# Kernel tuning notes

Hardware: AMD Instinct MI355X
Metric: run time of the kernel (lower is better)

The kernel has to match this reference:

```python
import jax, jax.numpy as jnp
import numpy as np

HIDDEN = 4096
NUM_HEADS = 32
NUM_KV_HEADS = 8
HEAD_DIM = 128
EPS = 1e-6
ROPE_THETA = 1000000.0
B, S = 4, 1024


def setup_inputs() -> dict:
    key = jax.random.key(0)
    ks = jax.random.split(key, 8)
    sd = 1.0 / np.sqrt(HIDDEN)
    return {
        "hidden_states": jax.random.normal(ks[0], (B, S, HIDDEN), jnp.float32),
        "positions": jnp.broadcast_to(jnp.arange(S, dtype=jnp.int32), (B, S)),
        "wq": jax.random.normal(ks[1], (HIDDEN, NUM_HEADS * HEAD_DIM), jnp.float32) * sd,
        "wk": jax.random.normal(ks[2], (HIDDEN, NUM_KV_HEADS * HEAD_DIM), jnp.float32) * sd,
        "wv": jax.random.normal(ks[3], (HIDDEN, NUM_KV_HEADS * HEAD_DIM), jnp.float32) * sd,
        "wo": jax.random.normal(ks[4], (NUM_HEADS * HEAD_DIM, HIDDEN), jnp.float32) * sd,
        "q_norm_scale": jnp.ones((HEAD_DIM,), jnp.float32),
        "k_norm_scale": jnp.ones((HEAD_DIM,), jnp.float32),
    }


def _rms_norm(x, scale):
    # per-head RMSNorm over last dim (head_dim)
    var = jnp.mean(jnp.square(x), axis=-1, keepdims=True)
    return x * jax.lax.rsqrt(var + EPS) * scale


def _rope_non_neox(x, positions):
    # x: [B, S, H, D]; non-neox (interleaved) RoPE over full head_dim
    inv_freq = 1.0 / (ROPE_THETA ** (jnp.arange(0, HEAD_DIM, 2, dtype=jnp.float32) / HEAD_DIM))
    freqs = positions.astype(jnp.float32)[..., None] * inv_freq  # [B, S, D/2]
    cos = jnp.cos(freqs)[:, :, None, :]  # [B, S, 1, D/2]
    sin = jnp.sin(freqs)[:, :, None, :]
    x1 = x[..., 0::2]
    x2 = x[..., 1::2]
    o1 = x1 * cos - x2 * sin
    o2 = x2 * cos + x1 * sin
    return jnp.stack([o1, o2], axis=-1).reshape(x.shape)


def reference(hidden_states, positions, wq, wk, wv, wo, q_norm_scale, k_norm_scale):
    b, s, _ = hidden_states.shape
    q = (hidden_states @ wq).reshape(b, s, NUM_HEADS, HEAD_DIM)
    k = (hidden_states @ wk).reshape(b, s, NUM_KV_HEADS, HEAD_DIM)
    v = (hidden_states @ wv).reshape(b, s, NUM_KV_HEADS, HEAD_DIM)

    q = _rms_norm(q, q_norm_scale)
    k = _rms_norm(k, k_norm_scale)

    q = _rope_non_neox(q, positions)
    k = _rope_non_neox(k, positions)

    # GQA: expand kv heads to match q heads
    group = NUM_HEADS // NUM_KV_HEADS
    k = jnp.repeat(k, group, axis=2)  # [B, S, NH, D]
    v = jnp.repeat(v, group, axis=2)

    scale = HEAD_DIM ** -0.5
    scores = jnp.einsum("bqhd,bkhd->bhqk", q, k) * scale  # [B, NH, S, S]
    causal = jnp.tril(jnp.ones((s, s), dtype=bool))
    scores = jnp.where(causal, scores, jnp.finfo(scores.dtype).min)
    probs = jax.nn.softmax(scores, axis=-1)
    attn = jnp.einsum("bhqk,bkhd->bqhd", probs, v).reshape(b, s, NUM_HEADS * HEAD_DIM)
    return attn @ wo
```

## Files before the change

### kernel.cpp

```cpp
#include <hip/hip_runtime.h>
#include <hip/hip_bf16.h>
#include <cstdint>

#define HIDDEN 4096
#define NQ 32
#define NKV 8
#define HD 128
#define BB 4
#define SS 1024
#define NTOK (BB*SS)
#define NQKV 6144

typedef __bf16 bf16x8 __attribute__((ext_vector_type(8)));
typedef float f32x4 __attribute__((ext_vector_type(4)));
typedef unsigned short u16;
typedef unsigned int u32;

__device__ __forceinline__ void gload_lds16(const void* g, void* l) {
  __builtin_amdgcn_global_load_lds((const __attribute__((address_space(1))) u32*)g,
                                   (__attribute__((address_space(3))) u32*)l, 16, 0, 0);
}

__device__ __forceinline__ u16 f2bf(float f) {
  u32 x = __float_as_uint(f);
  u32 r = x + 0x7fffu + ((x >> 16) & 1u);
  return (u16)(r >> 16);
}
__device__ __forceinline__ float bf2f(u16 x) {
  u32 v = ((u32)x) << 16;
  return __uint_as_float(v);
}

__global__ void cast_f32_bf16_k(const float4* __restrict__ in, ushort4* __restrict__ out, int n4)
{
  for (int i = blockIdx.x*blockDim.x + threadIdx.x; i < n4; i += gridDim.x*blockDim.x) {
    float4 v = in[i];
    ushort4 o;
    o.x = f2bf(v.x); o.y = f2bf(v.y); o.z = f2bf(v.z); o.w = f2bf(v.w);
    out[i] = o;
  }
}

__global__ __launch_bounds__(256) void transpose_cast(const float* __restrict__ in,
                                                      u16* __restrict__ out, int K, int N)
{
  __shared__ float tile[32][33];
  int n0 = blockIdx.x*32, k0 = blockIdx.y*32;
  int tx = threadIdx.x & 31, ty = threadIdx.x >> 5;
  #pragma unroll
  for (int i=0;i<4;i++) {
    int k = ty + i*8;
    tile[k][tx] = in[(size_t)(k0+k)*N + n0 + tx];
  }
  __syncthreads();
  #pragma unroll
  for (int i=0;i<4;i++) {
    int n = ty + i*8;
    out[(size_t)(n0+n)*K + k0 + tx] = f2bf(tile[tx][n]);
  }
}

__global__ void rope_tab_k(const int* __restrict__ pos, float2* __restrict__ tab)
{
  int i = blockIdx.x*256 + threadIdx.x;
  if (i >= NTOK*64) return;
  int t = i >> 6, j = i & 63;
  float p = (float)pos[t];
  const float l2t = 19.931568569324174f;
  float inv = exp2f(-(float)j * (l2t/64.0f));
  float f = p * inv;
  tab[i] = make_float2(cosf(f), sinf(f));
}

template<int BF16_OUT>
__global__ __launch_bounds__(512, 2) void gemm8p(const u16* __restrict__ A,
                                                 const u16* __restrict__ Bt,
                                                 void* __restrict__ Cv,
                                                 int M, int N, int K)
{
  __shared__ u16 lA[2][2][128*64];
  __shared__ u16 lB[2][2][128*64];
  const int m0 = blockIdx.y*256, n0 = blockIdx.x*256;
  const int tid = threadIdx.x;
  const int w = tid >> 6, l = tid & 63;
  const int wm = w >> 2, wn = w & 3;
  const int cl = l & 15, g4 = l >> 4;
  const int sr = l >> 3;
  const int sg = (l & 7) ^ sr;
  const u16* Ab = A  + (size_t)m0*K;
  const u16* Bb = Bt + (size_t)n0*K;

  f32x4 acc[8][4] = {};
  const int nt = K >> 6;

#define STG_A(buf, half, kt) do { \
    gload_lds16(Ab + (size_t)((half)*128 +      w*8 + sr)*K + (kt)*64 + sg*8, &lA[buf][half][(     w*8)*64]); \
    gload_lds16(Ab + (size_t)((half)*128 + 64 + w*8 + sr)*K + (kt)*64 + sg*8, &lA[buf][half][(64 + w*8)*64]); \
  } while(0)
#define STG_B(buf, half, kt) do { \
    gload_lds16(Bb + (size_t)((half)*128 +      w*8 + sr)*K + (kt)*64 + sg*8, &lB[buf][half][(     w*8)*64]); \
    gload_lds16(Bb + (size_t)((half)*128 + 64 + w*8 + sr)*K + (kt)*64 + sg*8, &lB[buf][half][(64 + w*8)*64]); \
  } while(0)

#define RD_A(dst, buf, half) \
    _Pragma("unroll") for (int fi=0;fi<4;fi++) { \
      const int ra = (wm*64 + fi*16 + cl)*64; \
      _Pragma("unroll") for (int kk=0;kk<2;kk++) \
        dst[fi][kk] = *(const bf16x8*)&lA[buf][half][ra + (((kk*4+g4) ^ (cl&7)))*8]; \
    }
#define RD_B(dst, buf, half) \
    _Pragma("unroll") for (int fj=0;fj<2;fj++) { \
      const int rb = (wn*32 + fj*16 + cl)*64; \
      _Pragma("unroll") for (int kk=0;kk<2;kk++) \
        dst[fj][kk] = *(const bf16x8*)&lB[buf][half][rb + (((kk*4+g4) ^ (cl&7)))*8]; \
    }
#define MFMA_Q(ai, aj, afrag, bfrag) \
    __builtin_amdgcn_s_setprio(1); \
    _Pragma("unroll") for (int fi=0;fi<4;fi++) \
      _Pragma("unroll") for (int fj=0;fj<2;fj++) \
        _Pragma("unroll") for (int kk=0;kk<2;kk++) \
          acc[(ai)+fi][(aj)+fj] = __builtin_amdgcn_mfma_f32_16x16x32_bf16(afrag[fi][kk], bfrag[fj][kk], acc[(ai)+fi][(aj)+fj], 0,0,0); \
    __builtin_amdgcn_s_setprio(0);
#define BAR() { __builtin_amdgcn_s_barrier(); __builtin_amdgcn_sched_barrier(0); }

  STG_A(0,0,0); STG_B(0,0,0); STG_A(0,1,0); STG_B(0,1,0);
  asm volatile("s_waitcnt vmcnt(4)" ::: "memory");
  BAR();

  for (int t = 0; t < nt; ++t) {
    const int cur = t & 1, nxt = cur ^ 1;
    const int kn = t + 1;
    const bool pf = (kn < nt);
    bf16x8 aF[4][2], bL[2][2], bH[2][2];

    RD_A(aF, cur, 0);
    RD_B(bL, cur, 0);
    if (pf) STG_A(nxt, 0, kn);
    BAR();
    MFMA_Q(0, 0, aF, bL);
    if (pf) { asm volatile("s_waitcnt vmcnt(2)" ::: "memory"); }
    else    { asm volatile("s_waitcnt vmcnt(0)" ::: "memory"); }
    BAR();

    RD_B(bH, cur, 1);
    if (pf) STG_B(nxt, 0, kn);
    BAR();
    MFMA_Q(0, 2, aF, bH);
    BAR();

    RD_A(aF, cur, 1);
    if (pf) STG_A(nxt, 1, kn);
    BAR();
    MFMA_Q(4, 2, aF, bH);
    BAR();

    if (pf) STG_B(nxt, 1, kn);
    BAR();
    MFMA_Q(4, 0, aF, bL);
    if (pf) { asm volatile("s_waitcnt vmcnt(4)" ::: "memory"); }
    BAR();
  }
#undef STG_A
#undef STG_B
#undef RD_A
#undef RD_B
#undef MFMA_Q
#undef BAR

  #pragma unroll
  for (int am=0;am<8;am++)
    #pragma unroll
    for (int rg=0;rg<4;rg++) {
      const size_t row = m0 + (am>>2)*128 + wm*64 + (am&3)*16 + g4*4 + rg;
      #pragma unroll
      for (int an=0;an<4;an++) {
        const size_t col = n0 + (an>>1)*128 + wn*32 + (an&1)*16 + cl;
        if (BF16_OUT) ((u16*)Cv)[row*N + col] = f2bf(acc[am][an][rg]);
        else          ((float*)Cv)[row*N + col] = acc[am][an][rg];
      }
    }
}

__global__ __launch_bounds__(256) void norm_rope(u16* __restrict__ qkv,
                                                 const float* __restrict__ qsc,
                                                 const float* __restrict__ ksc,
                                                 const float2* __restrict__ tab)
{
  const int t = blockIdx.x;
  const int w = threadIdx.x >> 6, l = threadIdx.x & 63;
  const float2 cs = tab[t*64 + l];
  for (int slot = w; slot < 40; slot += 4) {
    const float* sc = (slot < 32) ? qsc : ksc;
    int col = (slot < 32) ? slot*HD : 4096 + (slot-32)*HD;
    u32* p = (u32*)(qkv + (size_t)t*NQKV + col) + l;
    u32 v = *p;
    float x0 = bf2f((u16)(v & 0xffff)), x1 = bf2f((u16)(v >> 16));
    float ss = x0*x0 + x1*x1;
    ss += __shfl_xor(ss, 1);  ss += __shfl_xor(ss, 2);  ss += __shfl_xor(ss, 4);
    ss += __shfl_xor(ss, 8);  ss += __shfl_xor(ss, 16); ss += __shfl_xor(ss, 32);
    float r = rsqrtf(ss * (1.0f/128.0f) + 1e-6f);
    float y0 = x0 * r * sc[2*l], y1 = x1 * r * sc[2*l+1];
    float o0 = y0*cs.x - y1*cs.y;
    float o1 = y1*cs.x + y0*cs.y;
    *p = (u32)f2bf(o0) | ((u32)f2bf(o1) << 16);
  }
}

__global__ __launch_bounds__(256) void v_transpose(const u16* __restrict__ qkv,
                                                   u16* __restrict__ vt)
{
  __shared__ u16 tile[32][136];
  const int s0 = blockIdx.x*32;
  const int z  = blockIdx.y;
  const int b = z >> 3, kvh = z & 7;
  const int tid = threadIdx.x;
  const int tr = tid >> 4, ln = tid & 15;
  const size_t base = ((size_t)b*SS)*NQKV + 5120 + (size_t)kvh*HD;
  #pragma unroll
  for (int i=0;i<2;i++) {
    int srow = tr + i*16;
    *(bf16x8*)&tile[srow][ln*8] =
        *(const bf16x8*)&qkv[base + (size_t)(s0+srow)*NQKV + ln*8];
  }
  __syncthreads();
  const int dr = tid >> 1, sh = (tid & 1)*16;
  u16 tmp[16];
  #pragma unroll
  for (int j=0;j<16;j++) tmp[j] = tile[sh+j][dr];
  u16* o = vt + ((size_t)z*HD + dr)*SS + s0 + sh;
  *(bf16x8*)o       = *(const bf16x8*)&tmp[0];
  *(bf16x8*)(o + 8) = *(const bf16x8*)&tmp[8];
}

__global__ __launch_bounds__(256, 2) void attn_fwd(const u16* __restrict__ qkv,
                                                   const u16* __restrict__ vt,
                                                   u16* __restrict__ out)
{
  __shared__ u16 Kb[2][64*128];
  __shared__ u16 Vb[2][128*64];
  __shared__ u16 Pl[4][16*64];
  const int qp = blockIdx.x, h = blockIdx.y, b = blockIdx.z;
  const int kvh = h >> 2;
  const int tid = threadIdx.x, w = tid >> 6, l = tid & 63;
  const int cl = l & 15, g4 = l >> 4;
  const float csc = 1.4426950408889634f * 0.08838834764831845f;
  const size_t kbase = ((size_t)b*SS)*NQKV + 4096 + (size_t)kvh*HD;
  const size_t vbase = ((size_t)b*8 + (size_t)kvh)*HD*SS;
  u16* Pw = &Pl[w][0];

  const int kr_l = l >> 4, kg_l = l & 15;
  const int vr_l = l >> 3, vg_l = l & 7;

  #pragma unroll
  for (int t = 0; t < 2; ++t) {
    const int qt = t ? (15 - qp) : qp;
    const int q0 = qt*64;

    bf16x8 qf[4];
    const size_t qrow = ((size_t)b*SS + q0 + w*16 + cl)*NQKV + h*HD;
    #pragma unroll
    for (int kk=0;kk<4;kk++) qf[kk] = *(const bf16x8*)&qkv[qrow + kk*32 + g4*8];

    f32x4 O[8] = {};
    float mrow[4] = {-INFINITY,-INFINITY,-INFINITY,-INFINITY};
    float srow[4] = {0.f,0.f,0.f,0.f};

    const int nch = qt + 1;

    #pragma unroll
    for (int i=0;i<4;i++) {
      int inst = w*4 + i;
      int r = inst*4 + kr_l;
      int g = kg_l ^ (r & 15);
      gload_lds16(qkv + kbase + (size_t)r*NQKV + g*8, &Kb[0][inst*512]);
      int d = inst*8 + vr_l;
      int gv = vg_l ^ (d & 7);
      gload_lds16(vt + vbase + (size_t)d*SS + gv*8, &Vb[0][inst*512]);
    }
    __syncthreads();
    int cur = 0;

    for (int ch = 0; ch < nch; ++ch) {
      const int kv0 = ch*64;
      if (ch + 1 < nch) {
        const size_t knext = kbase + (size_t)(kv0+64)*NQKV;
        const size_t vnext = vbase + (size_t)(kv0+64);
        u16* Kn = &Kb[cur^1][0];
        u16* Vn = &Vb[cur^1][0];
        #pragma unroll
        for (int i=0;i<4;i++) {
          int inst = w*4 + i;
          int r = inst*4 + kr_l;
          int g = kg_l ^ (r & 15);
          gload_lds16(qkv + knext + (size_t)r*NQKV + g*8, Kn + inst*512);
          int d = inst*8 + vr_l;
          int gv = vg_l ^ (d & 7);
          gload_lds16(vt + vnext + (size_t)d*SS + gv*8, Vn + inst*512);
        }
      }
      const u16* Kt  = &Kb[cur][0];
      const u16* Vtl = &Vb[cur][0];
      f32x4 s[4] = {};
      #pragma unroll
      for (int cc=0;cc<4;cc++) {
        const int kro = (cc*16+cl)*128;
        #pragma unroll
        for (int kk=0;kk<4;kk++) {
          bf16x8 kf = *(const bf16x8*)&Kt[kro + (((kk*4+g4) ^ cl))*8];
          s[cc] = __builtin_amdgcn_mfma_f32_16x16x32_bf16(qf[kk], kf, s[cc], 0,0,0);
        }
      }
      float alpha[4];
      #pragma unroll
      for (int rg=0; rg<4; ++rg) {
        const int qr = q0 + w*16 + g4*4 + rg;
        float sv[4];
        #pragma unroll
        for (int cc=0;cc<4;cc++) {
          sv[cc] = s[cc][rg]*csc;
          if (kv0 + cc*16 + cl > qr) sv[cc] = -INFINITY;
        }
        float mx = fmaxf(fmaxf(sv[0],sv[1]), fmaxf(sv[2],sv[3]));
        mx = fmaxf(mx, __shfl_xor(mx,1));
        mx = fmaxf(mx, __shfl_xor(mx,2));
        mx = fmaxf(mx, __shfl_xor(mx,4));
        mx = fmaxf(mx, __shfl_xor(mx,8));
        float mn = fmaxf(mrow[rg], mx);
        float al = exp2f(mrow[rg] - mn);
        mrow[rg] = mn;
        float p0 = exp2f(sv[0]-mn), p1 = exp2f(sv[1]-mn);
        float p2 = exp2f(sv[2]-mn), p3 = exp2f(sv[3]-mn);
        float ps = (p0+p1)+(p2+p3);
        ps += __shfl_xor(ps,1); ps += __shfl_xor(ps,2);
        ps += __shfl_xor(ps,4); ps += __shfl_xor(ps,8);
        srow[rg] = srow[rg]*al + ps;
        alpha[rg] = al;
        const int r = g4*4+rg;
        const int rs = r*64, rx = r&7;
        float pv[4] = {p0,p1,p2,p3};
        #pragma unroll
        for (int cc=0;cc<4;cc++) {
          int c = cc*16+cl;
          Pw[rs + (((c>>3) ^ rx))*8 + (c&7)] = f2bf(pv[cc]);
        }
      }
      #pragma unroll
      for (int dc=0;dc<8;dc++)
        #pragma unroll
        for (int rg=0;rg<4;rg++) O[dc][rg] *= alpha[rg];
      #pragma unroll
      for (int cc2=0;cc2<2;cc2++) {
        bf16x8 pf = *(const bf16x8*)&Pw[cl*64 + (((cc2*4+g4) ^ (cl&7)))*8];
        #pragma unroll
        for (int dc=0;dc<8;dc++) {
          bf16x8 vf = *(const bf16x8*)&Vtl[(dc*16+cl)*64 + (((cc2*4+g4) ^ (cl&7)))*8];
          O[dc] = __builtin_amdgcn_mfma_f32_16x16x32_bf16(pf, vf, O[dc], 0,0,0);
        }
      }
      __syncthreads();
      cur ^= 1;
    }
    #pragma unroll
    for (int rg=0;rg<4;rg++) {
      float inv = 1.0f / srow[rg];
      size_t ob = ((size_t)b*SS + q0 + w*16 + g4*4 + rg)*4096 + (size_t)h*HD;
      #pragma unroll
      for (int dc=0;dc<8;dc++)
        out[ob + dc*16 + cl] = f2bf(O[dc][rg]*inv);
    }
  }
}

extern "C" void kernel_launch(void* const* d_in, const int* in_sizes, int n_in,
                              void* d_out, int out_size, void* d_ws, size_t ws_size,
                              hipStream_t stream)
{
  const float* hid = (const float*)d_in[0];
  const int*   pos = (const int*)d_in[1];
  const float* wq  = (const float*)d_in[2];
  const float* wk  = (const float*)d_in[3];
  const float* wv  = (const float*)d_in[4];
  const float* wo  = (const float*)d_in[5];
  const float* qsc = (const float*)d_in[6];
  const float* ksc = (const float*)d_in[7];

  char* ws = (char*)d_ws;
  size_t off = 0;
  auto alloc = [&](size_t b) -> char* {
    char* p = ws + off;
    off = (off + b + 255) & ~(size_t)255;
    return p;
  };
  u16*    h_bf   = (u16*)   alloc((size_t)NTOK*HIDDEN*2);
  u16*    wqkv_t = (u16*)   alloc((size_t)NQKV*HIDDEN*2);
  u16*    wo_t   = (u16*)   alloc((size_t)HIDDEN*HIDDEN*2);
  u16*    qkv    = (u16*)   alloc((size_t)NTOK*NQKV*2);
  u16*    attn_o = (u16*)   alloc((size_t)NTOK*HIDDEN*2);
  u16*    vtb    = (u16*)   alloc((size_t)BB*NKV*HD*SS*2);
  float2* tab    = (float2*)alloc((size_t)NTOK*64*sizeof(float2));

  cast_f32_bf16_k<<<2048, 256, 0, stream>>>((const float4*)hid, (ushort4*)h_bf, NTOK*HIDDEN/4);
  transpose_cast<<<dim3(HIDDEN/32, HIDDEN/32), 256, 0, stream>>>(wq, wqkv_t, HIDDEN, HIDDEN);
  transpose_cast<<<dim3(1024/32,  HIDDEN/32), 256, 0, stream>>>(wk, wqkv_t + (size_t)4096*HIDDEN, HIDDEN, 1024);
  transpose_cast<<<dim3(1024/32,  HIDDEN/32), 256, 0, stream>>>(wv, wqkv_t + (size_t)5120*HIDDEN, HIDDEN, 1024);
  transpose_cast<<<dim3(HIDDEN/32, HIDDEN/32), 256, 0, stream>>>(wo, wo_t, HIDDEN, HIDDEN);
  rope_tab_k<<<NTOK*64/256, 256, 0, stream>>>(pos, tab);

  gemm8p<1><<<dim3(NQKV/256, NTOK/256), 512, 0, stream>>>(h_bf, wqkv_t, qkv, NTOK, NQKV, HIDDEN);
  norm_rope<<<NTOK, 256, 0, stream>>>(qkv, qsc, ksc, tab);
  v_transpose<<<dim3(SS/32, BB*NKV), 256, 0, stream>>>(qkv, vtb);
  attn_fwd<<<dim3(8, NQ, BB), 256, 0, stream>>>(qkv, vtb, attn_o);
  gemm8p<0><<<dim3(HIDDEN/256, NTOK/256), 512, 0, stream>>>(attn_o, wo_t, d_out, NTOK, HIDDEN, HIDDEN);
}
```

Before: 543.2 us.

## Deepen GEMM global-to-LDS prefetch to two k-tiles ahead

Restructures the bf16 GEMM main loop so loads for tile t+2 are issued into the current buffer halves as soon as they are consumed, with the first tile plus most of the second prefetched in the prologue. The vmcnt waits are rearranged so more loads stay in flight while the MFMAs run, aiming to hide more global memory latency. This relies on careful buffer-reuse ordering across barriers and adds more outstanding loads; a mistake in the ordering would cause races. The STG address math is also widened to size_t.

Measured after the change: 534.4 us. No clear change (-1.6%).

```diff
diff --git a/kernel.cpp b/kernel.cpp
--- a/kernel.cpp
+++ b/kernel.cpp
@@ -94,12 +94,12 @@
   const int nt = K >> 6;
 
 #define STG_A(buf, half, kt) do { \
-    gload_lds16(Ab + (size_t)((half)*128 +      w*8 + sr)*K + (kt)*64 + sg*8, &lA[buf][half][(     w*8)*64]); \
-    gload_lds16(Ab + (size_t)((half)*128 + 64 + w*8 + sr)*K + (kt)*64 + sg*8, &lA[buf][half][(64 + w*8)*64]); \
+    gload_lds16(Ab + (size_t)((half)*128 +      w*8 + sr)*K + (size_t)(kt)*64 + sg*8, &lA[buf][half][(     w*8)*64]); \
+    gload_lds16(Ab + (size_t)((half)*128 + 64 + w*8 + sr)*K + (size_t)(kt)*64 + sg*8, &lA[buf][half][(64 + w*8)*64]); \
   } while(0)
 #define STG_B(buf, half, kt) do { \
-    gload_lds16(Bb + (size_t)((half)*128 +      w*8 + sr)*K + (kt)*64 + sg*8, &lB[buf][half][(     w*8)*64]); \
-    gload_lds16(Bb + (size_t)((half)*128 + 64 + w*8 + sr)*K + (kt)*64 + sg*8, &lB[buf][half][(64 + w*8)*64]); \
+    gload_lds16(Bb + (size_t)((half)*128 +      w*8 + sr)*K + (size_t)(kt)*64 + sg*8, &lB[buf][half][(     w*8)*64]); \
+    gload_lds16(Bb + (size_t)((half)*128 + 64 + w*8 + sr)*K + (size_t)(kt)*64 + sg*8, &lB[buf][half][(64 + w*8)*64]); \
   } while(0)
 
 #define RD_A(dst, buf, half) \
@@ -123,41 +123,42 @@
     __builtin_amdgcn_s_setprio(0);
 #define BAR() { __builtin_amdgcn_s_barrier(); __builtin_amdgcn_sched_barrier(0); }
 
-  STG_A(0,0,0); STG_B(0,0,0); STG_A(0,1,0); STG_B(0,1,0);
-  asm volatile("s_waitcnt vmcnt(4)" ::: "memory");
+  STG_A(0,0,0); STG_B(0,0,0); STG_B(0,1,0); STG_A(0,1,0);
+  STG_A(1,0,1); STG_B(1,0,1); STG_B(1,1,1);
+  asm volatile("s_waitcnt vmcnt(6)" ::: "memory");
   BAR();
 
   for (int t = 0; t < nt; ++t) {
-    const int cur = t & 1, nxt = cur ^ 1;
-    const int kn = t + 1;
-    const bool pf = (kn < nt);
+    const int cur = t & 1;
     bf16x8 aF[4][2], bL[2][2], bH[2][2];
 
     RD_A(aF, cur, 0);
     RD_B(bL, cur, 0);
-    if (pf) STG_A(nxt, 0, kn);
+    if (t+1 < nt) STG_A(cur^1, 1, t+1);
     BAR();
     MFMA_Q(0, 0, aF, bL);
-    if (pf) { asm volatile("s_waitcnt vmcnt(2)" ::: "memory"); }
-    else    { asm volatile("s_waitcnt vmcnt(0)" ::: "memory"); }
     BAR();
 
     RD_B(bH, cur, 1);
-    if (pf) STG_B(nxt, 0, kn);
+    if (t+2 < nt) STG_A(cur, 0, t+2);
     BAR();
     MFMA_Q(0, 2, aF, bH);
     BAR();
 
     RD_A(aF, cur, 1);
-    if (pf) STG_A(nxt, 1, kn);
+    if (t+2 < nt) STG_B(cur, 0, t+2);
     BAR();
     MFMA_Q(4, 2, aF, bH);
     BAR();
 
-    if (pf) STG_B(nxt, 1, kn);
+    if (t+2 < nt) {
+      STG_B(cur, 1, t+2);
+      asm volatile("s_waitcnt vmcnt(6)" ::: "memory");
+    } else if (t+1 < nt) {
+      asm volatile("s_waitcnt vmcnt(0)" ::: "memory");
+    }
     BAR();
     MFMA_Q(4, 0, aF, bL);
-    if (pf) { asm volatile("s_waitcnt vmcnt(4)" ::: "memory"); }
     BAR();
   }
 #undef STG_A
```
